# Optimization experiments

Hardware: AMD Instinct MI355X
Metric: run time of the kernel (lower is better)

The kernel has to match this reference:

```python
import jax, jax.numpy as jnp
import numpy as np

N_NODES = 100000
N_EDGES = 1600000
D_FEAT = 512
HEADS = 8
UNITS1 = 8          # layer1: 8 heads x 8 units, concat -> 64
HIDDEN = HEADS * UNITS1
OUT_DIM = 16        # layer2: 8 heads x 16 units, avg -> 16
N_IDX = 10000
NEG_SLOPE = 0.2     # LeakyReLU slope used by GAT attention


def _gat_layer(x, edges, W, a_src, a_dst, merge):
    """One multi-head GAT layer.
    x: [N, F], edges: [E, 2] with (dst, src) columns,
    W: [F, H, U], a_src/a_dst: [H, U].
    """
    n = x.shape[0]
    dst = edges[:, 0]
    src = edges[:, 1]
    h = jnp.einsum('nf,fhu->nhu', x, W)                      # [N, H, U]
    # per-node attention score halves, then gather per edge (cheaper than
    # gathering full features first)
    s_src = jnp.einsum('nhu,hu->nh', h, a_src)               # [N, H]
    s_dst = jnp.einsum('nhu,hu->nh', h, a_dst)               # [N, H]
    e = s_dst[dst] + s_src[src]                              # [E, H]
    e = jnp.where(e > 0, e, NEG_SLOPE * e)                   # LeakyReLU
    # segment softmax over incoming edges of each dst node (stable)
    m = jax.ops.segment_max(e, dst, num_segments=n)          # [N, H]
    m = jnp.where(jnp.isfinite(m), m, 0.0)                   # empty segments
    ex = jnp.exp(e - m[dst])                                 # [E, H]
    denom = jax.ops.segment_sum(ex, dst, num_segments=n)     # [N, H]
    alpha = ex / jnp.maximum(denom[dst], 1e-9)               # [E, H]
    msg = h[src] * alpha[:, :, None]                         # [E, H, U]
    out = jax.ops.segment_sum(msg, dst, num_segments=n)      # [N, H, U]
    if merge == 'concat':
        return out.reshape(n, -1)                            # [N, H*U]
    return out.mean(axis=1)                                  # [N, U]


def setup_inputs() -> dict:
    key = jax.random.key(0)
    ks = jax.random.split(key, 9)
    node_states = jax.random.normal(ks[0], (N_NODES, D_FEAT), dtype=jnp.float32)
    edges = jax.random.randint(ks[1], (N_EDGES, 2), 0, N_NODES, dtype=jnp.int32).astype(jnp.int64)
    indices = jax.random.randint(ks[2], (N_IDX,), 0, N_NODES, dtype=jnp.int32).astype(jnp.int64)
    W1 = jax.random.normal(ks[3], (D_FEAT, HEADS, UNITS1), dtype=jnp.float32) / np.sqrt(D_FEAT)
    a1_src = jax.random.normal(ks[4], (HEADS, UNITS1), dtype=jnp.float32) / np.sqrt(UNITS1)
    a1_dst = jax.random.normal(ks[5], (HEADS, UNITS1), dtype=jnp.float32) / np.sqrt(UNITS1)
    W2 = jax.random.normal(ks[6], (HIDDEN, HEADS, OUT_DIM), dtype=jnp.float32) / np.sqrt(HIDDEN)
    a2_src = jax.random.normal(ks[7], (HEADS, OUT_DIM), dtype=jnp.float32) / np.sqrt(OUT_DIM)
    a2_dst = jax.random.normal(ks[8], (HEADS, OUT_DIM), dtype=jnp.float32) / np.sqrt(OUT_DIM)
    return {
        'node_states': node_states, 'edges': edges, 'indices': indices,
        'W1': W1, 'a1_src': a1_src, 'a1_dst': a1_dst,
        'W2': W2, 'a2_src': a2_src, 'a2_dst': a2_dst,
    }


def reference(node_states, edges, indices, W1, a1_src, a1_dst, W2, a2_src, a2_dst):
    # layer 1: concat merge + ELU nonlinearity (standard GAT hidden layer)
    x = _gat_layer(node_states, edges, W1, a1_src, a1_dst, merge='concat')
    x = jax.nn.elu(x)                                        # [N, 64]
    # layer 2: average merge, linear output logits
    out = _gat_layer(x, edges, W2, a2_src, a2_dst, merge='avg')  # [N, OUT_DIM]
    return jnp.take(out, indices, axis=0)                    # [N_IDX, OUT_DIM]
```

## Files before the change

kernel.cpp:

```cpp
#include <hip/hip_runtime.h>
#include <hip/hip_bf16.h>

#define NN 100000
#define NE 1600000
#define DF 512
#define NIDX 10000

#define NBKT 512
#define BKT_W 196
#define EDGES_PER_BKT_BLK 3125
#define GEMM1_NB 782

typedef __attribute__((ext_vector_type(8))) short short8v;
typedef __attribute__((ext_vector_type(4))) float float4v;

__device__ __forceinline__ float eluf(float x) { return x > 0.f ? x : expm1f(x); }
__device__ __forceinline__ float lrelu(float x) { return x > 0.f ? x : 0.2f * x; }
__device__ __forceinline__ ushort f2bf(float f) {
  __hip_bfloat16 b = __float2bfloat16(f);
  return *(ushort*)&b;
}

__device__ __forceinline__ void glds16(const void* gsrc, void* ldst) {
  __builtin_amdgcn_global_load_lds(
      (const __attribute__((address_space(1))) uint32_t*)(uintptr_t)gsrc,
      (__attribute__((address_space(3))) uint32_t*)(uintptr_t)ldst, 16, 0, 0);
}

__global__ __launch_bounds__(256) void prep_w_kernel(const float* __restrict__ W1,
                                                     ushort* __restrict__ Wt_hi, ushort* __restrict__ Wt_lo,
                                                     int* __restrict__ bkt_cnt) {
  if (blockIdx.x == 0) {
    bkt_cnt[threadIdx.x] = 0;
    bkt_cnt[threadIdx.x + 256] = 0;
  }
  int t = blockIdx.x * 256 + threadIdx.x;
  if (t >= DF * 64) return;
  int k = t >> 6, n = t & 63;
  float w = W1[t];
  ushort hi = f2bf(w);
  __hip_bfloat16 hb = *(__hip_bfloat16*)&hi;
  ushort lo = f2bf(w - __bfloat162float(hb));
  Wt_hi[(size_t)n * DF + k] = hi;
  Wt_lo[(size_t)n * DF + k] = lo;
}

#define BSTRIDE 40
__global__ __launch_bounds__(256) void gemm1_hist(const float* __restrict__ x,
                                                  const ushort* __restrict__ Wt_hi, const ushort* __restrict__ Wt_lo,
                                                  const float* __restrict__ a1s, const float* __restrict__ a1d,
                                                  ushort* __restrict__ h1b, float* __restrict__ s_src,
                                                  float* __restrict__ s_dst,
                                                  const int2* __restrict__ edges, int* __restrict__ bkt_cnt) {
  __shared__ __align__(16) char smem[53248];
  const int tid = threadIdx.x;

  if (blockIdx.x >= GEMM1_NB) {
    int* h = (int*)smem;
    h[tid] = 0; h[tid + 256] = 0;
    __syncthreads();
    const int b = blockIdx.x - GEMM1_NB;
    const int i0 = b * EDGES_PER_BKT_BLK;
    const int i1 = min(i0 + EDGES_PER_BKT_BLK, NE);
    for (int i = i0 + tid; i < i1; i += 256) atomicAdd(&h[edges[i].x / BKT_W], 1);
    __syncthreads();
    if (h[tid]) atomicAdd(&bkt_cnt[tid], h[tid]);
    if (h[tid + 256]) atomicAdd(&bkt_cnt[tid + 256], h[tid + 256]);
    return;
  }

  float* Abuf[2];
  Abuf[0] = (float*)smem;
  Abuf[1] = (float*)(smem + 16384);
  ushort* Bhi[2]; ushort* Blo[2];
  Bhi[0] = (ushort*)(smem + 32768);
  Blo[0] = Bhi[0] + 64 * BSTRIDE;
  Bhi[1] = Blo[0] + 64 * BSTRIDE;
  Blo[1] = Bhi[1] + 64 * BSTRIDE;
  float* Cs = (float*)smem;

  const int mb = blockIdx.x * 128;
  const int wave = tid >> 6, l = tid & 63;
  const int wm = wave * 32;
  const int lm = l & 15, kq = l >> 4, kg = kq * 8;

  float4v acc[2][4];
#pragma unroll
  for (int i = 0; i < 2; ++i)
#pragma unroll
    for (int j = 0; j < 4; ++j) acc[i][j] = (float4v){0.f, 0.f, 0.f, 0.f};

  size_t asrc[4];
#pragma unroll
  for (int i = 0; i < 4; ++i) {
    int g = mb + wm + 8 * i + (l >> 3);
    if (g > NN - 1) g = NN - 1;
    asrc[i] = (size_t)g * DF + (l & 7) * 4;
  }
  const int bn = tid & 63, bk = (tid >> 6) * 8;

  {
    uint4 rbh = *(const uint4*)&Wt_hi[(size_t)bn * DF + bk];
    uint4 rbl = *(const uint4*)&Wt_lo[(size_t)bn * DF + bk];
    asm volatile("" ::: "memory");
#pragma unroll
    for (int i = 0; i < 4; ++i)
      glds16(x + asrc[i], (char*)Abuf[0] + wave * 4096 + i * 1024);
    *(uint4*)&Bhi[0][bn * BSTRIDE + bk] = rbh;
    *(uint4*)&Blo[0][bn * BSTRIDE + bk] = rbl;
    asm volatile("s_waitcnt lgkmcnt(0)" ::: "memory");
    __builtin_amdgcn_s_barrier();
  }

  for (int ks = 0; ks < 16; ++ks) {
    const int k0 = ks * 32;
    const int cur = ks & 1;
    uint4 rbh, rbl;
    if (ks < 15) {
      rbh = *(const uint4*)&Wt_hi[(size_t)bn * DF + k0 + 32 + bk];
      rbl = *(const uint4*)&Wt_lo[(size_t)bn * DF + k0 + 32 + bk];
      asm volatile("" ::: "memory");
#pragma unroll
      for (int i = 0; i < 4; ++i)
        glds16(x + asrc[i] + k0 + 32, (char*)Abuf[cur ^ 1] + wave * 4096 + i * 1024);
      asm volatile("s_waitcnt vmcnt(6)" ::: "memory");
    } else {
      asm volatile("s_waitcnt vmcnt(0)" ::: "memory");
    }
    short8v ah[2], al[2];
#pragma unroll
    for (int mt = 0; mt < 2; ++mt) {
      const float* p = Abuf[cur] + wave * 1024 + (mt * 16 + lm) * 32 + kg;
      float4 f0 = *(const float4*)p;
      float4 f1 = *(const float4*)(p + 4);
      float f[8] = {f0.x, f0.y, f0.z, f0.w, f1.x, f1.y, f1.z, f1.w};
#pragma unroll
      for (int c = 0; c < 8; ++c) {
        uint u = __float_as_uint(f[c]);
        ah[mt][c] = (short)(u >> 16);
        float hf = __uint_as_float(u & 0xFFFF0000u);
        al[mt][c] = (short)(__float_as_uint(f[c] - hf) >> 16);
      }
    }
    short8v bh[4], bl[4];
#pragma unroll
    for (int nt = 0; nt < 4; ++nt) {
      bh[nt] = *(const short8v*)&Bhi[cur][(nt * 16 + lm) * BSTRIDE + kg];
      bl[nt] = *(const short8v*)&Blo[cur][(nt * 16 + lm) * BSTRIDE + kg];
    }
#pragma unroll
    for (int mt = 0; mt < 2; ++mt)
#pragma unroll
      for (int nt = 0; nt < 4; ++nt) {
        acc[mt][nt] = __builtin_amdgcn_mfma_f32_16x16x32_bf16(ah[mt], bh[nt], acc[mt][nt], 0, 0, 0);
        acc[mt][nt] = __builtin_amdgcn_mfma_f32_16x16x32_bf16(ah[mt], bl[nt], acc[mt][nt], 0, 0, 0);
        acc[mt][nt] = __builtin_amdgcn_mfma_f32_16x16x32_bf16(al[mt], bh[nt], acc[mt][nt], 0, 0, 0);
      }
    if (ks < 15) {
      *(uint4*)&Bhi[cur ^ 1][bn * BSTRIDE + bk] = rbh;
      *(uint4*)&Blo[cur ^ 1][bn * BSTRIDE + bk] = rbl;
      asm volatile("s_waitcnt lgkmcnt(0)" ::: "memory");
    }
    __builtin_amdgcn_s_barrier();
  }

  __syncthreads();

#pragma unroll
  for (int mt = 0; mt < 2; ++mt)
#pragma unroll
    for (int nt = 0; nt < 4; ++nt)
#pragma unroll
      for (int r = 0; r < 4; ++r)
        Cs[(wm + mt * 16 + kq * 4 + r) * 65 + nt * 16 + lm] = acc[mt][nt][r];
  __syncthreads();

  {
    int row = tid >> 1, c0 = (tid & 1) * 32;
    int g = mb + row;
    if (g < NN) {
      uint u[16];
#pragma unroll
      for (int j = 0; j < 16; ++j) {
        uint p0 = f2bf(Cs[row * 65 + c0 + 2 * j]);
        uint p1 = f2bf(Cs[row * 65 + c0 + 2 * j + 1]);
        u[j] = p0 | (p1 << 16);
      }
#pragma unroll
      for (int q = 0; q < 4; ++q)
        *(uint4*)&h1b[(size_t)g * 64 + c0 + 8 * q] = *(uint4*)&u[4 * q];
      int half = tid & 1;
      float4 ssv, ddv;
      float* ssp = &ssv.x;
      float* ddp = &ddv.x;
#pragma unroll
      for (int hq = 0; hq < 4; ++hq) {
        int hh = half * 4 + hq;
        float ss = 0.f, dd = 0.f;
#pragma unroll
        for (int u8 = 0; u8 < 8; ++u8) {
          float hv = Cs[row * 65 + hh * 8 + u8];
          ss = fmaf(hv, a1s[hh * 8 + u8], ss);
          dd = fmaf(hv, a1d[hh * 8 + u8], dd);
        }
        ssp[hq] = ss; ddp[hq] = dd;
      }
      *(float4*)&s_src[(size_t)g * 8 + half * 4] = ssv;
      *(float4*)&s_dst[(size_t)g * 8 + half * 4] = ddv;
    }
  }
}

__global__ __launch_bounds__(256) void gemm2_fused(const float* __restrict__ A, const float* __restrict__ B,
                                                   __hip_bfloat162* __restrict__ Cb,
                                                   const float* __restrict__ a2s, const float* __restrict__ a2d,
                                                   float* __restrict__ s_src, float* __restrict__ s_dst,
                                                   int M) {
  __shared__ float sm[6528];
  float* As = sm;
  float* Bs = sm + 32 * 68;
  const int tid = threadIdx.x;
  const int m0 = blockIdx.x * 64;
  const int tx = tid & 15, ty = tid >> 4;
  float acc[4][8] = {};
  for (int k0 = 0; k0 < 64; k0 += 32) {
    for (int j = tid; j < 512; j += 256) {
      int r = j >> 3, kq = j & 7;
      int row = m0 + r;
      float4 v = make_float4(0.f, 0.f, 0.f, 0.f);
      if (row < M) v = *(const float4*)&A[(size_t)row * 64 + k0 + kq * 4];
      v.x = eluf(v.x); v.y = eluf(v.y); v.z = eluf(v.z); v.w = eluf(v.w);
      As[(kq * 4 + 0) * 68 + r] = v.x; As[(kq * 4 + 1) * 68 + r] = v.y;
      As[(kq * 4 + 2) * 68 + r] = v.z; As[(kq * 4 + 3) * 68 + r] = v.w;
    }
    for (int j = tid; j < 1024; j += 256) {
      int kr = j >> 5, nq = j & 31;
      *(float4*)&Bs[kr * 136 + nq * 4] = *(const float4*)&B[(size_t)(k0 + kr) * 128 + nq * 4];
    }
    __syncthreads();
#pragma unroll
    for (int kk = 0; kk < 32; ++kk) {
      float4 a4 = *(const float4*)&As[kk * 68 + ty * 4];
      float4 b0 = *(const float4*)&Bs[kk * 136 + tx * 8];
      float4 b1 = *(const float4*)&Bs[kk * 136 + tx * 8 + 4];
      float av[4] = {a4.x, a4.y, a4.z, a4.w};
      float bv[8] = {b0.x, b0.y, b0.z, b0.w, b1.x, b1.y, b1.z, b1.w};
#pragma unroll
      for (int i = 0; i < 4; ++i)
#pragma unroll
        for (int jj = 0; jj < 8; ++jj)
          acc[i][jj] = fmaf(av[i], bv[jj], acc[i][jj]);
    }
    __syncthreads();
  }
  const int hx = tx >> 1, half8 = (tx & 1) * 8;
#pragma unroll
  for (int i = 0; i < 4; ++i) {
    int row = m0 + ty * 4 + i;
    float ss = 0.f, dd = 0.f;
#pragma unroll
    for (int c = 0; c < 8; ++c) {
      ss = fmaf(acc[i][c], a2s[hx * 16 + half8 + c], ss);
      dd = fmaf(acc[i][c], a2d[hx * 16 + half8 + c], dd);
    }
    ss += __shfl_xor(ss, 1, 64);
    dd += __shfl_xor(dd, 1, 64);
    if (row < M) {
      uint u[4];
#pragma unroll
      for (int q = 0; q < 4; ++q)
        u[q] = (uint)f2bf(acc[i][2 * q]) | ((uint)f2bf(acc[i][2 * q + 1]) << 16);
      *(uint4*)&Cb[(size_t)row * 64 + tx * 4] = *(uint4*)u;
      if ((tx & 1) == 0) {
        s_src[(size_t)row * 8 + hx] = ss;
        s_dst[(size_t)row * 8 + hx] = dd;
      }
    }
  }
}

__global__ __launch_bounds__(NBKT) void bkt_scan_kernel(const int* __restrict__ bkt_cnt, int* __restrict__ bkt_base,
                                                        int* __restrict__ bkt_cursor, int* __restrict__ row_off) {
  __shared__ int s[NBKT];
  int tid = threadIdx.x;
  int v = bkt_cnt[tid];
  s[tid] = v;
  __syncthreads();
  for (int off = 1; off < NBKT; off <<= 1) {
    int t = (tid >= off) ? s[tid - off] : 0;
    __syncthreads();
    s[tid] += t;
    __syncthreads();
  }
  int excl = s[tid] - v;
  bkt_base[tid] = excl;
  bkt_cursor[tid] = excl;
  if (tid == NBKT - 1) bkt_base[NBKT] = s[tid];
  if (tid == 0) row_off[NN] = NE;
}

__global__ __launch_bounds__(256) void bkt_reorder_kernel(const int2* __restrict__ edges, int* __restrict__ bkt_cursor,
                                                          uint* __restrict__ pairs) {
  __shared__ int h[NBKT];
  __shared__ int lbase[NBKT];
  __shared__ int cur[NBKT];
  const int tid = threadIdx.x;
  h[tid] = 0; h[tid + 256] = 0;
  __syncthreads();
  const int i0 = blockIdx.x * EDGES_PER_BKT_BLK;
  const int i1 = min(i0 + EDGES_PER_BKT_BLK, NE);
  for (int i = i0 + tid; i < i1; i += 256) atomicAdd(&h[edges[i].x / BKT_W], 1);
  __syncthreads();
#pragma unroll
  for (int q = 0; q < 2; ++q) {
    int b = tid + q * 256;
    int c = h[b];
    lbase[b] = c ? atomicAdd(&bkt_cursor[b], c) : 0;
    cur[b] = 0;
  }
  __syncthreads();
  for (int i = i0 + tid; i < i1; i += 256) {
    int2 e = edges[i];
    int bk = e.x / BKT_W;
    int r = atomicAdd(&cur[bk], 1);
    pairs[lbase[bk] + r] = ((uint)(e.x - bk * BKT_W) << 24) | (uint)e.y;
  }
}

__global__ __launch_bounds__(256) void bkt_build_kernel(const uint* __restrict__ pairs, const int* __restrict__ bkt_base,
                                                        int* __restrict__ row_off, int* __restrict__ ssrc) {
  __shared__ int hist[256];
  __shared__ int ts[256];
  __shared__ int cur[256];
  const int b = blockIdx.x, tid = threadIdx.x;
  const int d0 = b * BKT_W;
  if (d0 >= NN) return;
  const int nd = min(BKT_W, NN - d0);
  const int beg = bkt_base[b], end = bkt_base[b + 1];
  hist[tid] = 0;
  __syncthreads();
  for (int i = beg + tid; i < end; i += 256) atomicAdd(&hist[pairs[i] >> 24], 1);
  __syncthreads();
  int v = hist[tid];
  ts[tid] = v;
  __syncthreads();
  for (int off = 1; off < 256; off <<= 1) {
    int t = (tid >= off) ? ts[tid - off] : 0;
    __syncthreads();
    ts[tid] += t;
    __syncthreads();
  }
  int excl = ts[tid] - v;
  if (tid < nd) row_off[d0 + tid] = beg + excl;
  cur[tid] = beg + excl;
  __syncthreads();
  for (int i = beg + tid; i < end; i += 256) {
    uint p = pairs[i];
    int pos = atomicAdd(&cur[p >> 24], 1);
    ssrc[pos] = (int)(p & 0xFFFFFFu);
  }
}

__global__ __launch_bounds__(256) void agg1_kernel(const int* __restrict__ row_off, const int* __restrict__ srcs,
                                                   const float* __restrict__ s_src, const float* __restrict__ s_dst,
                                                   const __hip_bfloat16* __restrict__ hb, float* __restrict__ out, int n) {
  int wave = (blockIdx.x * 256 + threadIdx.x) >> 6;
  int lane = threadIdx.x & 63;
  if (wave >= n) return;
  int hh = lane >> 3;
  float sd = s_dst[(size_t)wave * 8 + hh];
  int beg = row_off[wave], end = row_off[wave + 1];
  float acc = 0.f, den = 0.f;
  int i = beg;
  for (; i + 8 <= end; i += 8) {
    int s[8];
#pragma unroll
    for (int j = 0; j < 8; ++j) s[j] = srcs[i + j];
    float e[8], hv[8];
#pragma unroll
    for (int j = 0; j < 8; ++j) e[j] = s_src[(size_t)s[j] * 8 + hh];
#pragma unroll
    for (int j = 0; j < 8; ++j) hv[j] = __bfloat162float(hb[(size_t)s[j] * 64 + lane]);
#pragma unroll
    for (int j = 0; j < 8; ++j) {
      float xj = __expf(lrelu(sd + e[j]));
      den += xj;
      acc = fmaf(xj, hv[j], acc);
    }
  }
  for (; i < end; ++i) {
    int s0 = srcs[i];
    float x0 = __expf(lrelu(sd + s_src[(size_t)s0 * 8 + hh]));
    den += x0;
    acc = fmaf(x0, __bfloat162float(hb[(size_t)s0 * 64 + lane]), acc);
  }
  out[(size_t)wave * 64 + lane] = acc / fmaxf(den, 1e-9f);
}

__global__ __launch_bounds__(256) void agg2_idx_kernel(const int* __restrict__ row_off, const int* __restrict__ srcs,
                                                       const float* __restrict__ s_src, const float* __restrict__ s_dst,
                                                       const __hip_bfloat162* __restrict__ h2b, const int* __restrict__ idx,
                                                       float* __restrict__ out, int ni) {
  int w = (blockIdx.x * 256 + threadIdx.x) >> 6;
  int lane = threadIdx.x & 63;
  if (w >= ni) return;
  int node = idx[w];
  int hh = lane >> 3, o2 = lane & 7;
  float sd = s_dst[(size_t)node * 8 + hh];
  int beg = row_off[node], end = row_off[node + 1];
  float a0 = 0.f, a1 = 0.f, den = 0.f;
  int i = beg;
  for (; i + 4 <= end; i += 4) {
    int s0 = srcs[i], s1 = srcs[i + 1], s2 = srcs[i + 2], s3 = srcs[i + 3];
    float e0 = s_src[(size_t)s0 * 8 + hh];
    float e1 = s_src[(size_t)s1 * 8 + hh];
    float e2 = s_src[(size_t)s2 * 8 + hh];
    float e3 = s_src[(size_t)s3 * 8 + hh];
    float2 v0 = __bfloat1622float2(h2b[(size_t)s0 * 64 + hh * 8 + o2]);
    float2 v1 = __bfloat1622float2(h2b[(size_t)s1 * 64 + hh * 8 + o2]);
    float2 v2 = __bfloat1622float2(h2b[(size_t)s2 * 64 + hh * 8 + o2]);
    float2 v3 = __bfloat1622float2(h2b[(size_t)s3 * 64 + hh * 8 + o2]);
    float x0 = __expf(lrelu(sd + e0));
    float x1 = __expf(lrelu(sd + e1));
    float x2 = __expf(lrelu(sd + e2));
    float x3 = __expf(lrelu(sd + e3));
    den += (x0 + x1) + (x2 + x3);
    a0 = fmaf(x0, v0.x, fmaf(x1, v1.x, fmaf(x2, v2.x, fmaf(x3, v3.x, a0))));
    a1 = fmaf(x0, v0.y, fmaf(x1, v1.y, fmaf(x2, v2.y, fmaf(x3, v3.y, a1))));
  }
  for (; i < end; ++i) {
    int s0 = srcs[i];
    float x0 = __expf(lrelu(sd + s_src[(size_t)s0 * 8 + hh]));
    float2 v0 = __bfloat1622float2(h2b[(size_t)s0 * 64 + hh * 8 + o2]);
    den += x0;
    a0 = fmaf(x0, v0.x, a0);
    a1 = fmaf(x0, v0.y, a1);
  }
  float r0 = a0 / fmaxf(den, 1e-9f);
  float r1 = a1 / fmaxf(den, 1e-9f);
  for (int m = 8; m < 64; m <<= 1) {
    r0 += __shfl_xor(r0, m, 64);
    r1 += __shfl_xor(r1, m, 64);
  }
  if (lane < 8) {
    float2 wv = make_float2(r0 * 0.125f, r1 * 0.125f);
    *(float2*)&out[(size_t)w * 16 + lane * 2] = wv;
  }
}

extern "C" void kernel_launch(void* const* d_in, const int* in_sizes, int n_in,
                              void* d_out, int out_size, void* d_ws, size_t ws_size,
                              hipStream_t stream) {
  const float* x   = (const float*)d_in[0];
  const int2* edges = (const int2*)d_in[1];
  const int* indices = (const int*)d_in[2];
  const float* W1  = (const float*)d_in[3];
  const float* a1s = (const float*)d_in[4];
  const float* a1d = (const float*)d_in[5];
  const float* W2  = (const float*)d_in[6];
  const float* a2s = (const float*)d_in[7];
  const float* a2d = (const float*)d_in[8];
  float* out = (float*)d_out;

  char* ws = (char*)d_ws;
  size_t off = 0;
  auto alloc = [&](size_t bytes) {
    void* p = ws + off;
    off = (off + bytes + 255) & ~(size_t)255;
    return p;
  };
  float* s1src = (float*)alloc((size_t)NN * 8 * 4);
  float* s1dst = (float*)alloc((size_t)NN * 8 * 4);
  float* out1  = (float*)alloc((size_t)NN * 64 * 4);
  ushort* h1b  = (ushort*)alloc((size_t)NN * 64 * 2);
  __hip_bfloat162* h2b = (__hip_bfloat162*)alloc((size_t)NN * 128 * 2);
  int* row_off = (int*)alloc(((size_t)NN + 1) * 4);
  int* ssrc    = (int*)alloc((size_t)NE * 4);
  uint* pairs  = (uint*)alloc((size_t)NE * 4);
  ushort* Wt_hi = (ushort*)alloc((size_t)DF * 64 * 2);
  ushort* Wt_lo = (ushort*)alloc((size_t)DF * 64 * 2);
  int* bkt_cnt    = (int*)alloc(NBKT * 4);
  int* bkt_base   = (int*)alloc((NBKT + 1) * 4);
  int* bkt_cursor = (int*)alloc(NBKT * 4);

  dim3 b256(256);
  prep_w_kernel<<<dim3((DF * 64 + 255) / 256), b256, 0, stream>>>(W1, Wt_hi, Wt_lo, bkt_cnt);
  gemm1_hist<<<dim3(GEMM1_NB + NBKT), b256, 0, stream>>>(x, Wt_hi, Wt_lo, a1s, a1d, h1b, s1src, s1dst,
                                                          edges, bkt_cnt);
  bkt_scan_kernel<<<dim3(1), dim3(NBKT), 0, stream>>>(bkt_cnt, bkt_base, bkt_cursor, row_off);
  bkt_reorder_kernel<<<dim3(NBKT), b256, 0, stream>>>(edges, bkt_cursor, pairs);
  bkt_build_kernel<<<dim3(NBKT), b256, 0, stream>>>(pairs, bkt_base, row_off, ssrc);
  agg1_kernel<<<dim3(NN / 4), b256, 0, stream>>>(row_off, ssrc, s1src, s1dst, (const __hip_bfloat16*)h1b, out1, NN);
  gemm2_fused<<<dim3((NN + 63) / 64), b256, 0, stream>>>(out1, W2, h2b, a2s, a2d, s1src, s1dst, NN);
  agg2_idx_kernel<<<dim3((NIDX * 64 + 255) / 256), b256, 0, stream>>>(row_off, ssrc, s1src, s1dst, h2b, indices, out, NIDX);
}
```

Before: 250.7 us.

## Split GEMM1 in halves and co-schedule with edge reorder and CSR build

The edge histogram moves into the W1 prep kernel, and GEMM1 is split into two launches. The first half runs alongside the bucket-reorder blocks and the second half alongside the CSR-build blocks. This hides the memory-bound graph preprocessing behind the compute-bound GEMM and removes two standalone kernel launches. In exchange, it adds a memset and mixes block types whose different shared-memory and register needs may limit occupancy.

```diff
diff --git a/kernel.cpp b/kernel.cpp
--- a/kernel.cpp
+++ b/kernel.cpp
@@ -10,6 +10,8 @@
 #define BKT_W 196
 #define EDGES_PER_BKT_BLK 3125
 #define GEMM1_NB 782
+#define GEMM1A 391
+#define GEMM1B (GEMM1_NB - GEMM1A)
 
 typedef __attribute__((ext_vector_type(8))) short short8v;
 typedef __attribute__((ext_vector_type(4))) float float4v;
@@ -27,15 +29,24 @@
       (__attribute__((address_space(3))) uint32_t*)(uintptr_t)ldst, 16, 0, 0);
 }
 
-__global__ __launch_bounds__(256) void prep_w_kernel(const float* __restrict__ W1,
-                                                     ushort* __restrict__ Wt_hi, ushort* __restrict__ Wt_lo,
-                                                     int* __restrict__ bkt_cnt) {
-  if (blockIdx.x == 0) {
-    bkt_cnt[threadIdx.x] = 0;
-    bkt_cnt[threadIdx.x + 256] = 0;
-  }
-  int t = blockIdx.x * 256 + threadIdx.x;
-  if (t >= DF * 64) return;
+__global__ __launch_bounds__(256) void prep_w_hist(const float* __restrict__ W1,
+                                                   ushort* __restrict__ Wt_hi, ushort* __restrict__ Wt_lo,
+                                                   const int2* __restrict__ edges, int* __restrict__ bkt_cnt) {
+  const int tid = threadIdx.x;
+  if (blockIdx.x >= 128) {
+    __shared__ int h[NBKT];
+    h[tid] = 0; h[tid + 256] = 0;
+    __syncthreads();
+    const int b = blockIdx.x - 128;
+    const int i0 = b * EDGES_PER_BKT_BLK;
+    const int i1 = min(i0 + EDGES_PER_BKT_BLK, NE);
+    for (int i = i0 + tid; i < i1; i += 256) atomicAdd(&h[edges[i].x / BKT_W], 1);
+    __syncthreads();
+    if (h[tid]) atomicAdd(&bkt_cnt[tid], h[tid]);
+    if (h[tid + 256]) atomicAdd(&bkt_cnt[tid + 256], h[tid + 256]);
+    return;
+  }
+  int t = blockIdx.x * 256 + tid;
   int k = t >> 6, n = t & 63;
   float w = W1[t];
   ushort hi = f2bf(w);
@@ -46,26 +57,77 @@
 }
 
 #define BSTRIDE 40
-__global__ __launch_bounds__(256) void gemm1_hist(const float* __restrict__ x,
-                                                  const ushort* __restrict__ Wt_hi, const ushort* __restrict__ Wt_lo,
-                                                  const float* __restrict__ a1s, const float* __restrict__ a1d,
-                                                  ushort* __restrict__ h1b, float* __restrict__ s_src,
-                                                  float* __restrict__ s_dst,
-                                                  const int2* __restrict__ edges, int* __restrict__ bkt_cnt) {
+template<int TAIL>
+__global__ __launch_bounds__(256) void gemm1_mix(const float* __restrict__ x,
+                                                 const ushort* __restrict__ Wt_hi, const ushort* __restrict__ Wt_lo,
+                                                 const float* __restrict__ a1s, const float* __restrict__ a1d,
+                                                 ushort* __restrict__ h1b, float* __restrict__ s_src,
+                                                 float* __restrict__ s_dst,
+                                                 int gemm_cnt, int gemm_off,
+                                                 const int2* __restrict__ edges, int* __restrict__ bkt_cursor,
+                                                 uint* __restrict__ pairs,
+                                                 const int* __restrict__ bkt_base, int* __restrict__ row_off,
+                                                 int* __restrict__ ssrc) {
   __shared__ __align__(16) char smem[53248];
   const int tid = threadIdx.x;
 
-  if (blockIdx.x >= GEMM1_NB) {
-    int* h = (int*)smem;
-    h[tid] = 0; h[tid + 256] = 0;
-    __syncthreads();
-    const int b = blockIdx.x - GEMM1_NB;
-    const int i0 = b * EDGES_PER_BKT_BLK;
-    const int i1 = min(i0 + EDGES_PER_BKT_BLK, NE);
-    for (int i = i0 + tid; i < i1; i += 256) atomicAdd(&h[edges[i].x / BKT_W], 1);
-    __syncthreads();
-    if (h[tid]) atomicAdd(&bkt_cnt[tid], h[tid]);
-    if (h[tid + 256]) atomicAdd(&bkt_cnt[tid + 256], h[tid + 256]);
+  if (blockIdx.x >= (unsigned)gemm_cnt) {
+    const int tb = blockIdx.x - gemm_cnt;
+    if (TAIL == 0) {
+      int* h = (int*)smem;
+      int* lbase = h + NBKT;
+      int* cur = lbase + NBKT;
+      h[tid] = 0; h[tid + 256] = 0;
+      __syncthreads();
+      const int i0 = tb * EDGES_PER_BKT_BLK;
+      const int i1 = min(i0 + EDGES_PER_BKT_BLK, NE);
+      for (int i = i0 + tid; i < i1; i += 256) atomicAdd(&h[edges[i].x / BKT_W], 1);
+      __syncthreads();
+#pragma unroll
+      for (int q = 0; q < 2; ++q) {
+        int b = tid + q * 256;
+        int c = h[b];
+        lbase[b] = c ? atomicAdd(&bkt_cursor[b], c) : 0;
+        cur[b] = 0;
+      }
+      __syncthreads();
+      for (int i = i0 + tid; i < i1; i += 256) {
+        int2 e = edges[i];
+        int bk = e.x / BKT_W;
+        int r = atomicAdd(&cur[bk], 1);
+        pairs[lbase[bk] + r] = ((uint)(e.x - bk * BKT_W) << 24) | (uint)e.y;
+      }
+    } else {
+      int* hist = (int*)smem;
+      int* ts = hist + 256;
+      int* cur = ts + 256;
+      const int d0 = tb * BKT_W;
+      if (d0 >= NN) return;
+      const int nd = min(BKT_W, NN - d0);
+      const int beg = bkt_base[tb], end = bkt_base[tb + 1];
+      hist[tid] = 0;
+      __syncthreads();
+      for (int i = beg + tid; i < end; i += 256) atomicAdd(&hist[pairs[i] >> 24], 1);
+      __syncthreads();
+      int v = hist[tid];
+      ts[tid] = v;
+      __syncthreads();
+      for (int off = 1; off < 256; off <<= 1) {
+        int t2 = (tid >= off) ? ts[tid - off] : 0;
+        __syncthreads();
+        ts[tid] += t2;
+        __syncthreads();
+      }
+      int excl = ts[tid] - v;
+      if (tid < nd) row_off[d0 + tid] = beg + excl;
+      cur[tid] = beg + excl;
+      __syncthreads();
+      for (int i = beg + tid; i < end; i += 256) {
+        uint p = pairs[i];
+        int pos = atomicAdd(&cur[p >> 24], 1);
+        ssrc[pos] = (int)(p & 0xFFFFFFu);
+      }
+    }
     return;
   }
 
@@ -79,7 +141,7 @@
   Blo[1] = Bhi[1] + 64 * BSTRIDE;
   float* Cs = (float*)smem;
 
-  const int mb = blockIdx.x * 128;
+  const int mb = (gemm_off + blockIdx.x) * 128;
   const int wave = tid >> 6, l = tid & 63;
   const int wm = wave * 32;
   const int lm = l & 15, kq = l >> 4, kg = kq * 8;
@@ -209,6 +271,26 @@
       *(float4*)&s_dst[(size_t)g * 8 + half * 4] = ddv;
     }
   }
+}
+
+__global__ __launch_bounds__(NBKT) void bkt_scan_kernel(const int* __restrict__ bkt_cnt, int* __restrict__ bkt_base,
+                                                        int* __restrict__ bkt_cursor, int* __restrict__ row_off) {
+  __shared__ int s[NBKT];
+  int tid = threadIdx.x;
+  int v = bkt_cnt[tid];
+  s[tid] = v;
+  __syncthreads();
+  for (int off = 1; off < NBKT; off <<= 1) {
+    int t = (tid >= off) ? s[tid - off] : 0;
+    __syncthreads();
+    s[tid] += t;
+    __syncthreads();
+  }
+  int excl = s[tid] - v;
+  bkt_base[tid] = excl;
+  bkt_cursor[tid] = excl;
+  if (tid == NBKT - 1) bkt_base[NBKT] = s[tid];
+  if (tid == 0) row_off[NN] = NE;
 }
 
 __global__ __launch_bounds__(256) void gemm2_fused(const float* __restrict__ A, const float* __restrict__ B,
@@ -276,88 +358,6 @@
         s_dst[(size_t)row * 8 + hx] = dd;
       }
     }
-  }
-}
-
-__global__ __launch_bounds__(NBKT) void bkt_scan_kernel(const int* __restrict__ bkt_cnt, int* __restrict__ bkt_base,
-                                                        int* __restrict__ bkt_cursor, int* __restrict__ row_off) {
-  __shared__ int s[NBKT];
-  int tid = threadIdx.x;
-  int v = bkt_cnt[tid];
-  s[tid] = v;
-  __syncthreads();
-  for (int off = 1; off < NBKT; off <<= 1) {
-    int t = (tid >= off) ? s[tid - off] : 0;
-    __syncthreads();
-    s[tid] += t;
-    __syncthreads();
-  }
-  int excl = s[tid] - v;
-  bkt_base[tid] = excl;
-  bkt_cursor[tid] = excl;
-  if (tid == NBKT - 1) bkt_base[NBKT] = s[tid];
-  if (tid == 0) row_off[NN] = NE;
-}
-
-__global__ __launch_bounds__(256) void bkt_reorder_kernel(const int2* __restrict__ edges, int* __restrict__ bkt_cursor,
-                                                          uint* __restrict__ pairs) {
-  __shared__ int h[NBKT];
-  __shared__ int lbase[NBKT];
-  __shared__ int cur[NBKT];
-  const int tid = threadIdx.x;
-  h[tid] = 0; h[tid + 256] = 0;
-  __syncthreads();
-  const int i0 = blockIdx.x * EDGES_PER_BKT_BLK;
-  const int i1 = min(i0 + EDGES_PER_BKT_BLK, NE);
-  for (int i = i0 + tid; i < i1; i += 256) atomicAdd(&h[edges[i].x / BKT_W], 1);
-  __syncthreads();
-#pragma unroll
-  for (int q = 0; q < 2; ++q) {
-    int b = tid + q * 256;
-    int c = h[b];
-    lbase[b] = c ? atomicAdd(&bkt_cursor[b], c) : 0;
-    cur[b] = 0;
-  }
-  __syncthreads();
-  for (int i = i0 + tid; i < i1; i += 256) {
-    int2 e = edges[i];
-    int bk = e.x / BKT_W;
-    int r = atomicAdd(&cur[bk], 1);
-    pairs[lbase[bk] + r] = ((uint)(e.x - bk * BKT_W) << 24) | (uint)e.y;
-  }
-}
-
-__global__ __launch_bounds__(256) void bkt_build_kernel(const uint* __restrict__ pairs, const int* __restrict__ bkt_base,
-                                                        int* __restrict__ row_off, int* __restrict__ ssrc) {
-  __shared__ int hist[256];
-  __shared__ int ts[256];
-  __shared__ int cur[256];
-  const int b = blockIdx.x, tid = threadIdx.x;
-  const int d0 = b * BKT_W;
-  if (d0 >= NN) return;
-  const int nd = min(BKT_W, NN - d0);
-  const int beg = bkt_base[b], end = bkt_base[b + 1];
-  hist[tid] = 0;
-  __syncthreads();
-  for (int i = beg + tid; i < end; i += 256) atomicAdd(&hist[pairs[i] >> 24], 1);
-  __syncthreads();
-  int v = hist[tid];
-  ts[tid] = v;
-  __syncthreads();
-  for (int off = 1; off < 256; off <<= 1) {
-    int t = (tid >= off) ? ts[tid - off] : 0;
-    __syncthreads();
-    ts[tid] += t;
-    __syncthreads();
-  }
-  int excl = ts[tid] - v;
-  if (tid < nd) row_off[d0 + tid] = beg + excl;
-  cur[tid] = beg + excl;
-  __syncthreads();
-  for (int i = beg + tid; i < end; i += 256) {
-    uint p = pairs[i];
-    int pos = atomicAdd(&cur[p >> 24], 1);
-    ssrc[pos] = (int)(p & 0xFFFFFFu);
   }
 }
 
@@ -483,13 +483,17 @@
   int* bkt_base   = (int*)alloc((NBKT + 1) * 4);
   int* bkt_cursor = (int*)alloc(NBKT * 4);
 
+  hipMemsetAsync(bkt_cnt, 0, NBKT * 4, stream);
+
   dim3 b256(256);
-  prep_w_kernel<<<dim3((DF * 64 + 255) / 256), b256, 0, stream>>>(W1, Wt_hi, Wt_lo, bkt_cnt);
-  gemm1_hist<<<dim3(GEMM1_NB + NBKT), b256, 0, stream>>>(x, Wt_hi, Wt_lo, a1s, a1d, h1b, s1src, s1dst,
-                                                          edges, bkt_cnt);
+  prep_w_hist<<<dim3(128 + NBKT), b256, 0, stream>>>(W1, Wt_hi, Wt_lo, edges, bkt_cnt);
   bkt_scan_kernel<<<dim3(1), dim3(NBKT), 0, stream>>>(bkt_cnt, bkt_base, bkt_cursor, row_off);
-  bkt_reorder_kernel<<<dim3(NBKT), b256, 0, stream>>>(edges, bkt_cursor, pairs);
-  bkt_build_kernel<<<dim3(NBKT), b256, 0, stream>>>(pairs, bkt_base, row_off, ssrc);
+  gemm1_mix<0><<<dim3(GEMM1A + NBKT), b256, 0, stream>>>(x, Wt_hi, Wt_lo, a1s, a1d, h1b, s1src, s1dst,
+                                                         GEMM1A, 0, edges, bkt_cursor, pairs,
+                                                         bkt_base, row_off, ssrc);
+  gemm1_mix<1><<<dim3(GEMM1B + NBKT), b256, 0, stream>>>(x, Wt_hi, Wt_lo, a1s, a1d, h1b, s1src, s1dst,
+                                                         GEMM1B, GEMM1A, edges, bkt_cursor, pairs,
+                                                         bkt_base, row_off, ssrc);
   agg1_kernel<<<dim3(NN / 4), b256, 0, stream>>>(row_off, ssrc, s1src, s1dst, (const __hip_bfloat16*)h1b, out1, NN);
   gemm2_fused<<<dim3((NN + 63) / 64), b256, 0, stream>>>(out1, W2, h2b, a2s, a2d, s1src, s1dst, NN);
   agg2_idx_kernel<<<dim3((NIDX * 64 + 255) / 256), b256, 0, stream>>>(row_off, ssrc, s1src, s1dst, h2b, indices, out, NIDX);
```

Result: no change. 245.9 us, median of 2 (-1.9%).
